# Kernel tuning notes

Measured on AMD Instinct MI355X. Metric: run time of the kernel, lower is better.

Reference implementation:

```python
import jax, jax.numpy as jnp
import numpy as np

N = 50000          # nodes
E = 1600000        # edges (avg degree 32)
D_IN = 128
D_OUT = 128
NEG_SLOPE = 0.01   # F.leaky_relu default (module ignores its negative_slope attr)


def setup_inputs() -> dict:
    key = jax.random.key(0)
    k = jax.random.split(key, 7)
    h = jax.random.normal(k[0], (N, D_IN), dtype=jnp.float32)
    embedding = jax.random.normal(k[1], (N, D_OUT), dtype=jnp.float32)
    # params (xavier-ish scaling)
    W_lin = jax.random.normal(k[2], (D_OUT, D_IN), dtype=jnp.float32) * (2.0 / (D_IN + D_OUT)) ** 0.5
    w_fc = jax.random.normal(k[3], (1, 2 * D_OUT), dtype=jnp.float32) * (2.0 / (2 * D_OUT + 1)) ** 0.5
    w_emb = jax.random.normal(k[4], (1, 2 * D_OUT), dtype=jnp.float32) * (2.0 / (2 * D_OUT + 1)) ** 0.5
    src = jax.random.randint(k[5], (E,), 0, N, dtype=jnp.int64 if jax.config.jax_enable_x64 else jnp.int32)
    dst = jax.random.randint(k[6], (E,), 0, N, dtype=jnp.int64 if jax.config.jax_enable_x64 else jnp.int32)
    return {"h": h, "embedding": embedding, "W_lin": W_lin, "w_fc": w_fc,
            "w_emb": w_emb, "src": src, "dst": dst}


def reference(h, embedding, W_lin, w_fc, w_emb, src, dst):
    n = h.shape[0]
    d = W_lin.shape[0]
    # z = lin(h): [N, out]
    z = h @ W_lin.T
    # attn_fc(cat(z_src, z_dst)) + attn_embed(cat(e_src, e_dst)) split into per-node
    # scalar scores so we gather [E] scalars instead of materializing [E, 2*out].
    s_fc_src = z @ w_fc[0, :d]            # [N]
    s_fc_dst = z @ w_fc[0, d:]            # [N]
    s_em_src = embedding @ w_emb[0, :d]   # [N]
    s_em_dst = embedding @ w_emb[0, d:]   # [N]
    a = (s_fc_src + s_em_src)[src] + (s_fc_dst + s_em_dst)[dst]   # [E]
    e = jnp.where(a > 0, a, NEG_SLOPE * a)  # leaky_relu, slope 0.01
    # segment softmax over incoming edges of each dst node
    m = jax.ops.segment_max(e, dst, num_segments=n)               # [N]
    e_exp = jnp.exp(e - m[dst])                                   # [E]
    denom = jax.ops.segment_sum(e_exp, dst, num_segments=n)       # [N]
    alpha = e_exp / denom[dst]                                    # [E]
    # weighted neighbor aggregation: h_out[v] = sum_{(u->v)} alpha * z[u]
    h_out = jax.ops.segment_sum(alpha[:, None] * z[src], dst, num_segments=n)
    return h_out
```

## Files before the change

kernel.cpp:

```cpp
#include <hip/hip_runtime.h>
#include <hip/hip_bf16.h>

#define D 128
#define BSH 7
#define BDST 128
#define NCHK 512
#define CHCAP 3200
#define CAPB 5120
#define SL 8

typedef __attribute__((ext_vector_type(8))) short short8;
typedef __attribute__((ext_vector_type(4))) float f32x4;
typedef __attribute__((ext_vector_type(2))) float f32x2;

__device__ __forceinline__ unsigned short f2bf(float f) {
  unsigned u = __float_as_uint(f);
  unsigned r = (u + 0x7FFFu + ((u >> 16) & 1u)) >> 16;
  return (unsigned short)r;
}

__global__ __launch_bounds__(256) void k_wconv(const float* __restrict__ W,
                                               unsigned short* __restrict__ Wb) {
  const int i = blockIdx.x * 256 + threadIdx.x;
  float4 f = ((const float4*)W)[i];
  ushort4 o;
  o.x = f2bf(f.x); o.y = f2bf(f.y); o.z = f2bf(f.z); o.w = f2bf(f.w);
  ((ushort4*)Wb)[i] = o;
}

__global__ __launch_bounds__(256) void k_combo(
    const float* __restrict__ h, const unsigned short* __restrict__ Wb,
    const float* __restrict__ w_fc, const float* __restrict__ emb,
    const float* __restrict__ w_emb, unsigned* __restrict__ zd,
    float* __restrict__ a_src, float* __restrict__ a_dst,
    const int* __restrict__ src, const int* __restrict__ dst,
    int* __restrict__ bincur, unsigned* __restrict__ binrec,
    int n, int E, int NB, int CHSZ) {
  __shared__ unsigned recbuf[CHCAP];
  __shared__ int hl[512], gbase[512], loff[512], lcur[512];
  __shared__ int sh[256];
  __shared__ float sfs[4][16], sfd[4][16];
  const int tid = threadIdx.x;

  if ((int)blockIdx.x < NCHK) {
    const int c = blockIdx.x;
    const int beg = c * CHSZ, end = min(beg + CHSZ, E);
    const int cnt = end - beg;
    for (int i = tid; i < 512; i += 256) { hl[i] = 0; lcur[i] = 0; }
    __syncthreads();
    for (int i = beg + tid; i < end; i += 256) atomicAdd(&hl[dst[i] >> BSH], 1);
    __syncthreads();
    for (int b = tid; b < NB; b += 256) {
      int cb = hl[b];
      gbase[b] = cb > 0 ? atomicAdd(&bincur[b], cb) : 0;
    }
    int v0 = hl[2 * tid], v1 = hl[2 * tid + 1];
    int s = v0 + v1;
    sh[tid] = s;
    __syncthreads();
    for (int off = 1; off < 256; off <<= 1) {
      int a = (tid >= off) ? sh[tid - off] : 0;
      __syncthreads();
      sh[tid] += a;
      __syncthreads();
    }
    int base = sh[tid] - s;
    loff[2 * tid] = base;
    loff[2 * tid + 1] = base + v0;
    __syncthreads();
    for (int i = beg + tid; i < end; i += 256) {
      int d = dst[i];
      int b = d >> BSH;
      unsigned r = ((unsigned)src[i] << 16) | (unsigned)d;
      int lp = atomicAdd(&lcur[b], 1);
      recbuf[loff[b] + lp] = r;
    }
    __syncthreads();
    for (int i = tid; i < cnt; i += 256) {
      unsigned r = recbuf[i];
      int b = (int)(r & 0xFFFFu) >> BSH;
      binrec[(size_t)b * CAPB + gbase[b] + (i - loff[b])] = r;
    }
    return;
  }

  const int lane = tid & 63;
  const int wid = tid >> 6;
  const int m0 = (blockIdx.x - NCHK) * 64 + wid * 16;
  if (m0 >= n) return;
  const int c = lane & 15;
  const int g = lane >> 4;

  int arow = m0 + c;
  if (arow >= n) arow = n - 1;
  const float4* hrow = (const float4*)(h + (size_t)arow * 128);

  short8 afr[4];
#pragma unroll
  for (int s = 0; s < 4; ++s) {
    float4 f0 = hrow[8 * s + 2 * g];
    float4 f1 = hrow[8 * s + 2 * g + 1];
    short8 a;
    a[0] = (short)f2bf(f0.x); a[1] = (short)f2bf(f0.y);
    a[2] = (short)f2bf(f0.z); a[3] = (short)f2bf(f0.w);
    a[4] = (short)f2bf(f1.x); a[5] = (short)f2bf(f1.y);
    a[6] = (short)f2bf(f1.z); a[7] = (short)f2bf(f1.w);
    afr[s] = a;
  }

  f32x4 acc[8];
#pragma unroll
  for (int t = 0; t < 8; ++t) acc[t] = (f32x4){0.f, 0.f, 0.f, 0.f};

#pragma unroll
  for (int s = 0; s < 4; ++s) {
#pragma unroll
    for (int t = 0; t < 8; ++t) {
      short8 b = *(const short8*)(Wb + ((size_t)(t * 16 + c) * 128 + 32 * s + 8 * g));
      acc[t] = __builtin_amdgcn_mfma_f32_16x16x32_bf16(afr[s], b, acc[t], 0, 0, 0);
    }
  }

  float wfs[8], wfd[8];
#pragma unroll
  for (int t = 0; t < 8; ++t) {
    wfs[t] = w_fc[t * 16 + c];
    wfd[t] = w_fc[128 + t * 16 + c];
  }

  const int rbase = m0 + 4 * g;
#pragma unroll
  for (int r = 0; r < 4; ++r) {
    const int row = rbase + r;
    if (row < n) {
#pragma unroll
      for (int tp = 0; tp < 4; ++tp) {
        unsigned dw = ((unsigned)f2bf(acc[tp + 4][r]) << 16) | (unsigned)f2bf(acc[tp][r]);
        zd[(size_t)row * 64 + tp * 16 + c] = dw;
      }
    }
    float ps = 0.f, pd = 0.f;
#pragma unroll
    for (int t = 0; t < 8; ++t) {
      ps += acc[t][r] * wfs[t];
      pd += acc[t][r] * wfd[t];
    }
#pragma unroll
    for (int off = 1; off < 16; off <<= 1) {
      ps += __shfl_xor(ps, off, 64);
      pd += __shfl_xor(pd, off, 64);
    }
    if (c == 0) {
      sfs[wid][4 * g + r] = ps;
      sfd[wid][4 * g + r] = pd;
    }
  }
  __syncthreads();

  const int nloc = lane >> 2;
  const int qc = lane & 3;
  const int node2 = m0 + nloc;
  float es = 0.f, ed = 0.f;
  if (node2 < n) {
    const float4* er = (const float4*)(emb + (size_t)node2 * 128 + qc * 32);
    const float4* wsp = (const float4*)(w_emb + qc * 32);
    const float4* wdp = (const float4*)(w_emb + 128 + qc * 32);
#pragma unroll
    for (int j = 0; j < 8; ++j) {
      float4 e4 = er[j], s4 = wsp[j], d4 = wdp[j];
      es += e4.x * s4.x + e4.y * s4.y + e4.z * s4.z + e4.w * s4.w;
      ed += e4.x * d4.x + e4.y * d4.y + e4.z * d4.z + e4.w * d4.w;
    }
  }
  es += __shfl_xor(es, 1, 64); es += __shfl_xor(es, 2, 64);
  ed += __shfl_xor(ed, 1, 64); ed += __shfl_xor(ed, 2, 64);
  if (qc == 0 && node2 < n) {
    a_src[node2] = es + sfs[wid][nloc];
    a_dst[node2] = ed + sfd[wid][nloc];
  }
}

__global__ __launch_bounds__(256) void k_build(const unsigned* __restrict__ binrec,
                                               const int* __restrict__ bincur,
                                               int2* __restrict__ row2,
                                               int* __restrict__ csr, int n) {
  __shared__ int hist[BDST * SL];
  __shared__ int excl[BDST * SL];
  __shared__ int sh[256];
  const int tid = threadIdx.x, b = blockIdx.x;
  const int cntb = bincur[b];
  const unsigned* rb = binrec + (size_t)b * CAPB;
  const int base = b * CAPB;

  for (int k = tid; k < BDST * SL; k += 256) hist[k] = 0;
  __syncthreads();
  for (int i = tid; i < cntb; i += 256) {
    unsigned r = rb[i];
    int dl = r & (BDST - 1);
    int sv = (int)(r >> 16);
    atomicAdd(&hist[dl * SL + (sv >> 13)], 1);
  }
  __syncthreads();
  const int k0 = tid * 4;
  int v4[4], s = 0;
#pragma unroll
  for (int j = 0; j < 4; ++j) { v4[j] = hist[k0 + j]; s += v4[j]; }
  sh[tid] = s;
  __syncthreads();
  for (int off = 1; off < 256; off <<= 1) {
    int a = (tid >= off) ? sh[tid - off] : 0;
    __syncthreads();
    sh[tid] += a;
    __syncthreads();
  }
  int e0 = sh[tid] - s;
#pragma unroll
  for (int j = 0; j < 4; ++j) { excl[k0 + j] = e0; e0 += v4[j]; }
  __syncthreads();
  if (tid < BDST) {
    int bg = excl[tid * SL];
    int en = (tid == BDST - 1) ? cntb : excl[(tid + 1) * SL];
    int v = b * BDST + tid;
    if (v < n) row2[v] = make_int2(base + bg, base + en);
  }
  __syncthreads();
  for (int i = tid; i < cntb; i += 256) {
    unsigned r = rb[i];
    int dl = r & (BDST - 1);
    int sv = (int)(r >> 16);
    int pos = base + atomicAdd(&excl[dl * SL + (sv >> 13)], 1);
    csr[pos] = sv;
  }
}

__global__ __launch_bounds__(256) void k_agg(const unsigned* __restrict__ zd,
                                             const float* __restrict__ a_src,
                                             const float* __restrict__ a_dst,
                                             const int2* __restrict__ row2,
                                             const int* __restrict__ csr,
                                             float* __restrict__ out, int n) {
  const int lane = threadIdx.x & 63;
  const int grp = lane >> 4;
  const int sub = lane & 15;
  const int v = blockIdx.x * 4 + (threadIdx.x >> 6);
  if (v >= n) return;
  const int2 be = row2[v];
  const int beg = be.x, end = be.y;
  const float adv = a_dst[v];

  f32x2 acc2[4];
#pragma unroll
  for (int j = 0; j < 4; ++j) acc2[j] = (f32x2){0.f, 0.f};
  float ews = 0.f;

#pragma unroll 4
  for (int i = beg + grp; i < end; i += 4) {
    const int u = csr[i];
    const float a = a_src[u] + adv;
    const float e = a > 0.f ? a : 0.01f * a;
    const float ew = __expf(e);
    const uint4 zz = ((const uint4*)zd)[(size_t)u * 16 + sub];
    ews += ew;
    const f32x2 ew2 = {ew, ew};
    f32x2 z0 = {__uint_as_float(zz.x << 16), __uint_as_float(zz.x & 0xffff0000u)};
    f32x2 z1 = {__uint_as_float(zz.y << 16), __uint_as_float(zz.y & 0xffff0000u)};
    f32x2 z2 = {__uint_as_float(zz.z << 16), __uint_as_float(zz.z & 0xffff0000u)};
    f32x2 z3 = {__uint_as_float(zz.w << 16), __uint_as_float(zz.w & 0xffff0000u)};
    acc2[0] += ew2 * z0;
    acc2[1] += ew2 * z1;
    acc2[2] += ew2 * z2;
    acc2[3] += ew2 * z3;
  }

#pragma unroll
  for (int off = 16; off <= 32; off <<= 1) {
    ews += __shfl_xor(ews, off, 64);
#pragma unroll
    for (int j = 0; j < 4; ++j) {
      acc2[j][0] += __shfl_xor(acc2[j][0], off, 64);
      acc2[j][1] += __shfl_xor(acc2[j][1], off, 64);
    }
  }

  if (grp == 0) {
    const float inv = (end > beg) ? 1.f / ews : 0.f;
    float4 olo = make_float4(acc2[0][0] * inv, acc2[1][0] * inv, acc2[2][0] * inv, acc2[3][0] * inv);
    float4 ohi = make_float4(acc2[0][1] * inv, acc2[1][1] * inv, acc2[2][1] * inv, acc2[3][1] * inv);
    ((float4*)out)[(size_t)v * 32 + sub] = olo;
    ((float4*)out)[(size_t)v * 32 + 16 + sub] = ohi;
  }
}

extern "C" void kernel_launch(void* const* d_in, const int* in_sizes, int n_in,
                              void* d_out, int out_size, void* d_ws, size_t ws_size,
                              hipStream_t stream) {
  const float* h = (const float*)d_in[0];
  const float* emb = (const float*)d_in[1];
  const float* W = (const float*)d_in[2];
  const float* wfc = (const float*)d_in[3];
  const float* wemb = (const float*)d_in[4];
  const int* src = (const int*)d_in[5];
  const int* dst = (const int*)d_in[6];
  const int n = in_sizes[0] / D;
  const int E = in_sizes[5];
  const int NB = (n + BDST - 1) >> BSH;
  const int CHSZ = (E + NCHK - 1) / NCHK;
  const int NLIN = (n + 63) / 64;

  char* ws = (char*)d_ws;
  size_t off = 0;
  auto alloc = [&](size_t bytes) {
    void* p = ws + off;
    off = (off + bytes + 255) & ~(size_t)255;
    return p;
  };
  unsigned* zd = (unsigned*)alloc((size_t)n * 64 * 4);
  unsigned short* Wb = (unsigned short*)alloc(D * D * 2);
  float* a_src = (float*)alloc((size_t)n * 4);
  float* a_dst = (float*)alloc((size_t)n * 4);
  int* bincur = (int*)alloc((size_t)NB * 4);
  int2* row2 = (int2*)alloc((size_t)n * 8);
  unsigned* binrec = (unsigned*)alloc((size_t)NB * CAPB * 4);
  int* csr = (int*)alloc((size_t)NB * CAPB * 4);
  (void)off;
  (void)ws_size;

  (void)hipMemsetAsync(bincur, 0, (size_t)NB * 4, stream);
  k_wconv<<<(D * D / 4 + 255) / 256, 256, 0, stream>>>(W, Wb);
  k_combo<<<NCHK + NLIN, 256, 0, stream>>>(h, Wb, wfc, emb, wemb, zd, a_src, a_dst,
                                           src, dst, bincur, binrec, n, E, NB, CHSZ);
  k_build<<<NB, 256, 0, stream>>>(binrec, bincur, row2, csr, n);
  k_agg<<<(n + 3) / 4, 256, 0, stream>>>(zd, a_src, a_dst, row2, csr, (float*)d_out, n);
}
```

Measured before the change: 126.5 us.

## Precompute edge weights in CSR build, fold memset into wconv, rebalance chunks

Moves the per-edge leaky-relu and exp computation from the aggregation kernel into the CSR build kernel, storing (src, weight) pairs so aggregation no longer does a dependent a_src gather. The memset of bin counters is folded into the weight-conversion kernel to drop a separate launch. The chunk count for binning is doubled with halved per-chunk capacity. The CSR array doubles in size, adding write and read traffic, and the build kernel takes on the random a_src gathers.

```diff
diff --git a/kernel.cpp b/kernel.cpp
--- a/kernel.cpp
+++ b/kernel.cpp
@@ -4,8 +4,8 @@
 #define D 128
 #define BSH 7
 #define BDST 128
-#define NCHK 512
-#define CHCAP 3200
+#define NCHK 1024
+#define CHCAP 1600
 #define CAPB 5120
 #define SL 8
 
@@ -20,8 +20,10 @@
 }
 
 __global__ __launch_bounds__(256) void k_wconv(const float* __restrict__ W,
-                                               unsigned short* __restrict__ Wb) {
+                                               unsigned short* __restrict__ Wb,
+                                               int* __restrict__ bincur, int NB) {
   const int i = blockIdx.x * 256 + threadIdx.x;
+  if (i < NB) bincur[i] = 0;
   float4 f = ((const float4*)W)[i];
   ushort4 o;
   o.x = f2bf(f.x); o.y = f2bf(f.y); o.z = f2bf(f.z); o.w = f2bf(f.w);
@@ -182,17 +184,24 @@
 
 __global__ __launch_bounds__(256) void k_build(const unsigned* __restrict__ binrec,
                                                const int* __restrict__ bincur,
+                                               const float* __restrict__ a_src,
+                                               const float* __restrict__ a_dst,
                                                int2* __restrict__ row2,
-                                               int* __restrict__ csr, int n) {
+                                               int2* __restrict__ csr2, int n) {
   __shared__ int hist[BDST * SL];
   __shared__ int excl[BDST * SL];
   __shared__ int sh[256];
+  __shared__ float adl[BDST];
   const int tid = threadIdx.x, b = blockIdx.x;
   const int cntb = bincur[b];
   const unsigned* rb = binrec + (size_t)b * CAPB;
   const int base = b * CAPB;
 
   for (int k = tid; k < BDST * SL; k += 256) hist[k] = 0;
+  if (tid < BDST) {
+    int v = b * BDST + tid;
+    adl[tid] = (v < n) ? a_dst[v] : 0.f;
+  }
   __syncthreads();
   for (int i = tid; i < cntb; i += 256) {
     unsigned r = rb[i];
@@ -228,16 +237,17 @@
     unsigned r = rb[i];
     int dl = r & (BDST - 1);
     int sv = (int)(r >> 16);
+    float a = a_src[sv] + adl[dl];
+    float e = a > 0.f ? a : 0.01f * a;
+    float ew = __expf(e);
     int pos = base + atomicAdd(&excl[dl * SL + (sv >> 13)], 1);
-    csr[pos] = sv;
+    csr2[pos] = make_int2(sv, __float_as_int(ew));
   }
 }
 
 __global__ __launch_bounds__(256) void k_agg(const unsigned* __restrict__ zd,
-                                             const float* __restrict__ a_src,
-                                             const float* __restrict__ a_dst,
                                              const int2* __restrict__ row2,
-                                             const int* __restrict__ csr,
+                                             const int2* __restrict__ csr2,
                                              float* __restrict__ out, int n) {
   const int lane = threadIdx.x & 63;
   const int grp = lane >> 4;
@@ -246,7 +256,6 @@
   if (v >= n) return;
   const int2 be = row2[v];
   const int beg = be.x, end = be.y;
-  const float adv = a_dst[v];
 
   f32x2 acc2[4];
 #pragma unroll
@@ -255,11 +264,9 @@
 
 #pragma unroll 4
   for (int i = beg + grp; i < end; i += 4) {
-    const int u = csr[i];
-    const float a = a_src[u] + adv;
-    const float e = a > 0.f ? a : 0.01f * a;
-    const float ew = __expf(e);
-    const uint4 zz = ((const uint4*)zd)[(size_t)u * 16 + sub];
+    const int2 e2 = csr2[i];
+    const float ew = __int_as_float(e2.y);
+    const uint4 zz = ((const uint4*)zd)[(size_t)e2.x * 16 + sub];
     ews += ew;
     const f32x2 ew2 = {ew, ew};
     f32x2 z0 = {__uint_as_float(zz.x << 16), __uint_as_float(zz.x & 0xffff0000u)};
@@ -321,14 +328,13 @@
   int* bincur = (int*)alloc((size_t)NB * 4);
   int2* row2 = (int2*)alloc((size_t)n * 8);
   unsigned* binrec = (unsigned*)alloc((size_t)NB * CAPB * 4);
-  int* csr = (int*)alloc((size_t)NB * CAPB * 4);
+  int2* csr2 = (int2*)alloc((size_t)NB * CAPB * 8);
   (void)off;
   (void)ws_size;
 
-  (void)hipMemsetAsync(bincur, 0, (size_t)NB * 4, stream);
-  k_wconv<<<(D * D / 4 + 255) / 256, 256, 0, stream>>>(W, Wb);
+  k_wconv<<<(D * D / 4 + 255) / 256, 256, 0, stream>>>(W, Wb, bincur, NB);
   k_combo<<<NCHK + NLIN, 256, 0, stream>>>(h, Wb, wfc, emb, wemb, zd, a_src, a_dst,
                                            src, dst, bincur, binrec, n, E, NB, CHSZ);
-  k_build<<<NB, 256, 0, stream>>>(binrec, bincur, row2, csr, n);
-  k_agg<<<(n + 3) / 4, 256, 0, stream>>>(zd, a_src, a_dst, row2, csr, (float*)d_out, n);
-}
+  k_build<<<NB, 256, 0, stream>>>(binrec, bincur, a_src, a_dst, row2, csr2, n);
+  k_agg<<<(n + 3) / 4, 256, 0, stream>>>(zd, row2, csr2, (float*)d_out, n);
+}
```

Measured after the change: 140.5 us. +11.0%, slower.
